# Kernel tuning notes

Measured on AMD Instinct MI355X. Metric: run time of the kernel, lower is better.

## Reference

```python
import jax, jax.numpy as jnp
import numpy as np
from jax import lax

EPS = 0.1
MAX_ITER = 100
THRESH = 0.1


def setup_inputs() -> dict:
    key = jax.random.key(0)
    k1, k2, k3 = jax.random.split(key, 3)
    x = jax.random.normal(k1, (128, 512, 3), dtype=jnp.float32)
    y = jax.random.normal(k2, (128, 512, 3), dtype=jnp.float32)
    species = jax.random.uniform(k3, (512, 8), dtype=jnp.float32)
    return {"x": x, "y": y, "species": species}


def _cost_matrix(x, y, species):
    # periodic displacement: round(dx) - dx, squared L2 over coord dim
    dx = x[:, :, None, :] - y[:, None, :, :]          # (N, P1, P2, D)
    dper = jnp.round(dx) - dx
    dist_sqr = jnp.sum(jnp.abs(dper) ** 2, axis=-1)   # (N, P1, P2)
    C = dist_sqr * jnp.abs(1.0 / (species @ species.T) + 1e-5)  # broadcast (P,P)
    return C, dist_sqr


def _sinkhorn(C):
    N, P1, P2 = C.shape
    mu = jnp.full((N, P1), 1.0 / P1, dtype=C.dtype)
    nu = jnp.full((N, P2), 1.0 / P2, dtype=C.dtype)

    def M(u, v):
        # (-C + u_i + v_j) / eps
        return (-C + u[..., :, None] + v[..., None, :]) / EPS

    def step(carry, _):
        u, v, done = carry
        u_new = EPS * (jnp.log(mu + 1e-8) - jax.nn.logsumexp(M(u, v), axis=-1)) + u
        v_new = EPS * (jnp.log(nu + 1e-8) - jax.nn.logsumexp(M(u_new, v), axis=-2)) + v
        err = jnp.mean(jnp.sum(jnp.abs(u_new - u), axis=-1))
        # torch loop breaks AFTER applying this iteration's update; freeze afterwards
        u_out = jnp.where(done, u, u_new)
        v_out = jnp.where(done, v, v_new)
        done_out = done | (err < THRESH)
        return (u_out, v_out, done_out), None

    init = (jnp.zeros_like(mu), jnp.zeros_like(nu), jnp.array(False))
    (u, v, _), _ = lax.scan(step, init, None, length=MAX_ITER)
    pi = jnp.exp(M(u, v))
    return pi


def reference(x, y, species):
    C, dist_sqr = _cost_matrix(x, y, species)
    pi = _sinkhorn(C)
    cost = jnp.sum(pi * C, axis=(-2, -1))  # (N,), reduction='none'
    return (cost, pi, C, dist_sqr)
```

## Files before the change

### kernel.cpp

```cpp
#include <hip/hip_runtime.h>
#include <hip/hip_cooperative_groups.h>

namespace cg = cooperative_groups;

#define NB    128
#define P     512
#define PP    262144
#define TOT   33554432
#define MAX_IT 100

#define SCR_K      0
#define SCR_W      16777216
#define SCR_CP     17039360
#define SCR_U      17563648
#define SCR_V      17629184
#define SCR_ERRP   17694720
#define SCR_FLOATS 17695744
#define DIST_KEEP  (TOT - SCR_FLOATS)

__device__ __forceinline__ float bfbits(unsigned u) {
  union { unsigned b; float f; } x; x.b = u; return x.f;
}

__global__ void prep_kernel(const float* __restrict__ species,
                            float* __restrict__ scr, float* __restrict__ cost) {
  int tid = blockIdx.x * 256 + threadIdx.x;
  if (tid < PP) {
    int i = tid >> 9, j = tid & (P - 1);
    const float* si = species + i * 8;
    const float* sj = species + j * 8;
    float g = 0.f;
#pragma unroll
    for (int k = 0; k < 8; ++k) g += si[k] * sj[k];
    scr[SCR_W + tid] = fabsf(1.0f / g + 1e-5f);
  }
  if (tid < NB * P) scr[SCR_U + tid] = 0.f;
  if (tid < NB) cost[tid] = 0.f;
}

__global__ void cmat_kernel(const float* __restrict__ x, const float* __restrict__ y,
                            const float* __restrict__ W,
                            unsigned short* __restrict__ K,
                            float* __restrict__ C, float* __restrict__ dist) {
  int g = blockIdx.x * 256 + threadIdx.x;
  int base = g << 2;
  int n = base >> 18;
  int r = base & (PP - 1);
  int i = r >> 9, j0 = r & (P - 1);
  const float* xp = x + ((n << 9) + i) * 3;
  float x0 = xp[0], x1 = xp[1], x2 = xp[2];
  const float* yp = y + ((n << 9) + j0) * 3;
  float4 w4 = *reinterpret_cast<const float4*>(W + r);
  float wv[4] = { w4.x, w4.y, w4.z, w4.w };
  float c[4], d[4];
  unsigned short kk[4];
#pragma unroll
  for (int q = 0; q < 4; ++q) {
    float dx = x0 - yp[q * 3 + 0];
    float dy = x1 - yp[q * 3 + 1];
    float dz = x2 - yp[q * 3 + 2];
    dx = rintf(dx) - dx; dy = rintf(dy) - dy; dz = rintf(dz) - dz;
    float ds = dx * dx + dy * dy + dz * dz;
    d[q] = ds;
    c[q] = ds * wv[q];
    float kf = __expf(-10.f * c[q]);
    unsigned b = __float_as_uint(kf);
    kk[q] = (unsigned short)((b + 0x7fffu + ((b >> 16) & 1u)) >> 16);
  }
  *reinterpret_cast<float4*>(C + base) = make_float4(c[0], c[1], c[2], c[3]);
  if (base < DIST_KEEP)
    *reinterpret_cast<float4*>(dist + base) = make_float4(d[0], d[1], d[2], d[3]);
  uint2 kp;
  kp.x = (unsigned)kk[0] | ((unsigned)kk[1] << 16);
  kp.y = (unsigned)kk[2] | ((unsigned)kk[3] << 16);
  *reinterpret_cast<uint2*>(K + base) = kp;
}

__global__ void tail_kernel(const float* __restrict__ x, const float* __restrict__ y,
                            float* __restrict__ dist) {
  int idx = DIST_KEEP + blockIdx.x * 256 + threadIdx.x;
  int n = idx >> 18;
  int r = idx & (PP - 1);
  int i = r >> 9, j = r & (P - 1);
  const float* xp = x + ((n << 9) + i) * 3;
  const float* yp = y + ((n << 9) + j) * 3;
  float ds = 0.f;
#pragma unroll
  for (int k = 0; k < 3; ++k) {
    float dd = xp[k] - yp[k];
    float per = rintf(dd) - dd;
    ds += per * per;
  }
  dist[idx] = ds;
}

__global__ __launch_bounds__(512, 4)
void sinkhorn_kernel(float* __restrict__ scr) {
  cg::grid_group grid = cg::this_grid();
  const unsigned short* Kus = (const unsigned short*)scr;
  float* u    = scr + SCR_U;
  float* cp   = scr + SCR_CP;
  float* errP = scr + SCR_ERRP;

  const int tid  = threadIdx.x;
  const int lane = tid & 63;
  const int wid  = tid >> 6;
  const int bid  = blockIdx.x;
  const int n    = bid >> 2;
  const int rb   = bid & 3;
  const int row0 = (n << 9) + (rb << 7);

  __shared__ float vLDS[512];
  __shared__ float colsum[512];
  __shared__ float red[512];
  __shared__ float wdu[8];

  vLDS[tid] = 0.f;
  __syncthreads();

  const float logmu = logf(1.0f / 512.0f + 1e-8f);

  for (int it = 0; it < MAX_IT; ++it) {
    const int buf = it & 1;
    float ev[8], colacc[8];
#pragma unroll
    for (int t = 0; t < 8; ++t) {
      ev[t] = __expf(10.f * vLDS[(lane << 3) + t]);
      colacc[t] = 0.f;
    }
    colsum[tid] = 0.f;
    __syncthreads();

    float myDu = 0.f;
#pragma unroll 2
    for (int r = 0; r < 16; ++r) {
      int row = row0 + (wid << 4) + r;
      const uint4* kp = reinterpret_cast<const uint4*>(Kus + ((size_t)row << 9) + (lane << 3));
      uint4 kw = *kp;
      float k[8];
      k[0] = bfbits(kw.x << 16); k[1] = bfbits(kw.x & 0xffff0000u);
      k[2] = bfbits(kw.y << 16); k[3] = bfbits(kw.y & 0xffff0000u);
      k[4] = bfbits(kw.z << 16); k[5] = bfbits(kw.z & 0xffff0000u);
      k[6] = bfbits(kw.w << 16); k[7] = bfbits(kw.w & 0xffff0000u);
      float s = 0.f;
#pragma unroll
      for (int t = 0; t < 8; ++t) s = fmaf(k[t], ev[t], s);
#pragma unroll
      for (int o = 32; o > 0; o >>= 1) s += __shfl_xor(s, o);
      float uo = u[row];
      float un = 0.1f * (logmu - __logf(s));
      myDu += fabsf(un - uo);
      if (lane == 0) u[row] = un;
      float eu = __expf(10.f * un);
#pragma unroll
      for (int t = 0; t < 8; ++t) colacc[t] = fmaf(k[t], eu, colacc[t]);
    }
#pragma unroll
    for (int t = 0; t < 8; ++t) atomicAdd(&colsum[(lane << 3) + t], colacc[t]);
    if (lane == 0) wdu[wid] = myDu;
    __syncthreads();

    cp[(buf << 18) + (n << 11) + (rb << 9) + tid] = colsum[tid];
    if (tid == 0) {
      float e = 0.f;
#pragma unroll
      for (int w = 0; w < 8; ++w) e += wdu[w];
      errP[(buf << 9) + bid] = e;
    }
    grid.sync();

    float sc = 0.f;
#pragma unroll
    for (int q = 0; q < 4; ++q) sc += cp[(buf << 18) + (n << 11) + (q << 9) + tid];
    float vc = 0.1f * (logmu - __logf(sc));

    red[tid] = errP[(buf << 9) + tid];
    __syncthreads();
#pragma unroll
    for (int o = 256; o > 0; o >>= 1) {
      if (tid < o) red[tid] += red[tid + o];
      __syncthreads();
    }
    float errTot = red[0];
    vLDS[tid] = vc;
    __syncthreads();
    if (errTot < 12.8f) break;
  }

  if (rb == 0) scr[SCR_V + (n << 9) + tid] = vLDS[tid];
}

__global__ __launch_bounds__(256)
void pi_kernel(const float* __restrict__ C, const float* __restrict__ scr,
               float* __restrict__ pi, float* __restrict__ cost) {
  int gid = blockIdx.x * 256 + threadIdx.x;
  int lane = threadIdx.x & 63;
  int row = gid >> 6;
  int n = row >> 9;
  int c0 = lane << 3;
  float uu = scr[SCR_U + row];
  const float* vp = scr + SCR_V + (n << 9) + c0;
  float4 va = *reinterpret_cast<const float4*>(vp);
  float4 vb = *reinterpret_cast<const float4*>(vp + 4);
  const float* Cr = C + ((size_t)row << 9) + c0;
  float4 ca = *reinterpret_cast<const float4*>(Cr);
  float4 cb = *reinterpret_cast<const float4*>(Cr + 4);
  float4 pa, pb;
  pa.x = __expf((uu + va.x - ca.x) * 10.f);
  pa.y = __expf((uu + va.y - ca.y) * 10.f);
  pa.z = __expf((uu + va.z - ca.z) * 10.f);
  pa.w = __expf((uu + va.w - ca.w) * 10.f);
  pb.x = __expf((uu + vb.x - cb.x) * 10.f);
  pb.y = __expf((uu + vb.y - cb.y) * 10.f);
  pb.z = __expf((uu + vb.z - cb.z) * 10.f);
  pb.w = __expf((uu + vb.w - cb.w) * 10.f);
  float* Pr = pi + ((size_t)row << 9) + c0;
  *reinterpret_cast<float4*>(Pr) = pa;
  *reinterpret_cast<float4*>(Pr + 4) = pb;
  float acc = pa.x * ca.x + pa.y * ca.y + pa.z * ca.z + pa.w * ca.w
            + pb.x * cb.x + pb.y * cb.y + pb.z * cb.z + pb.w * cb.w;
#pragma unroll
  for (int o = 32; o > 0; o >>= 1) acc += __shfl_xor(acc, o);
  __shared__ float ws[4];
  if (lane == 0) ws[threadIdx.x >> 6] = acc;
  __syncthreads();
  if (threadIdx.x == 0) atomicAdd(cost + n, ws[0] + ws[1] + ws[2] + ws[3]);
}

extern "C" void kernel_launch(void* const* d_in, const int* in_sizes, int n_in,
                              void* d_out, int out_size, void* d_ws, size_t ws_size,
                              hipStream_t stream) {
  const float* x = (const float*)d_in[0];
  const float* y = (const float*)d_in[1];
  const float* species = (const float*)d_in[2];

  float* out  = (float*)d_out;
  float* cost = out;
  float* pi   = out + 128;
  float* C    = pi + (size_t)TOT;
  float* dist = C + (size_t)TOT;
  float* scr  = dist + (size_t)DIST_KEEP;

  hipLaunchKernelGGL(prep_kernel, dim3(PP / 256), dim3(256), 0, stream,
                     species, scr, cost);
  hipLaunchKernelGGL(cmat_kernel, dim3(TOT / 4 / 256), dim3(256), 0, stream,
                     x, y, scr + SCR_W, (unsigned short*)scr, C, dist);

  void* args[] = { (void*)&scr };
  hipLaunchCooperativeKernel((void*)sinkhorn_kernel, dim3(512), dim3(512),
                             args, 0, stream);

  hipLaunchKernelGGL(pi_kernel, dim3(TOT / 8 / 256), dim3(256), 0, stream,
                     C, scr, pi, cost);
  hipLaunchKernelGGL(tail_kernel, dim3(SCR_FLOATS / 256), dim3(256), 0, stream,
                     x, y, dist);
}
```

Baseline: 437.0 us.

## Keep bf16 Gibbs kernel in registers during Sinkhorn, recompute cost in pi kernel

```diff
diff --git a/kernel.cpp b/kernel.cpp
--- a/kernel.cpp
+++ b/kernel.cpp
@@ -9,13 +9,15 @@
 #define TOT   33554432
 #define MAX_IT 100
 
-#define SCR_K      0
-#define SCR_W      16777216
-#define SCR_CP     17039360
-#define SCR_U      17563648
-#define SCR_V      17629184
-#define SCR_ERRP   17694720
-#define SCR_FLOATS 17695744
+#define SCR_W      0
+#define SCR_X      262144
+#define SCR_Y      458752
+#define SCR_CP     655360
+#define SCR_U      1179648
+#define SCR_V      1245184
+#define SCR_ERRP   1310720
+#define SCR_DONE   1311744
+#define SCR_FLOATS 1312000
 #define DIST_KEEP  (TOT - SCR_FLOATS)
 
 __device__ __forceinline__ float bfbits(unsigned u) {
@@ -23,6 +25,7 @@
 }
 
 __global__ void prep_kernel(const float* __restrict__ species,
+                            const float* __restrict__ x, const float* __restrict__ y,
                             float* __restrict__ scr, float* __restrict__ cost) {
   int tid = blockIdx.x * 256 + threadIdx.x;
   if (tid < PP) {
@@ -34,13 +37,17 @@
     for (int k = 0; k < 8; ++k) g += si[k] * sj[k];
     scr[SCR_W + tid] = fabsf(1.0f / g + 1e-5f);
   }
+  if (tid < NB * P * 3) {
+    scr[SCR_X + tid] = x[tid];
+    scr[SCR_Y + tid] = y[tid];
+  }
   if (tid < NB * P) scr[SCR_U + tid] = 0.f;
   if (tid < NB) cost[tid] = 0.f;
+  if (tid == 0) scr[SCR_DONE] = 0.f;
 }
 
 __global__ void cmat_kernel(const float* __restrict__ x, const float* __restrict__ y,
                             const float* __restrict__ W,
-                            unsigned short* __restrict__ K,
                             float* __restrict__ C, float* __restrict__ dist) {
   int g = blockIdx.x * 256 + threadIdx.x;
   int base = g << 2;
@@ -53,7 +60,6 @@
   float4 w4 = *reinterpret_cast<const float4*>(W + r);
   float wv[4] = { w4.x, w4.y, w4.z, w4.w };
   float c[4], d[4];
-  unsigned short kk[4];
 #pragma unroll
   for (int q = 0; q < 4; ++q) {
     float dx = x0 - yp[q * 3 + 0];
@@ -63,17 +69,10 @@
     float ds = dx * dx + dy * dy + dz * dz;
     d[q] = ds;
     c[q] = ds * wv[q];
-    float kf = __expf(-10.f * c[q]);
-    unsigned b = __float_as_uint(kf);
-    kk[q] = (unsigned short)((b + 0x7fffu + ((b >> 16) & 1u)) >> 16);
   }
   *reinterpret_cast<float4*>(C + base) = make_float4(c[0], c[1], c[2], c[3]);
   if (base < DIST_KEEP)
     *reinterpret_cast<float4*>(dist + base) = make_float4(d[0], d[1], d[2], d[3]);
-  uint2 kp;
-  kp.x = (unsigned)kk[0] | ((unsigned)kk[1] << 16);
-  kp.y = (unsigned)kk[2] | ((unsigned)kk[3] << 16);
-  *reinterpret_cast<uint2*>(K + base) = kp;
 }
 
 __global__ void tail_kernel(const float* __restrict__ x, const float* __restrict__ y,
@@ -94,10 +93,142 @@
   dist[idx] = ds;
 }
 
+__global__ __launch_bounds__(256, 2)
+void sink_b(float* __restrict__ scr) {
+  cg::grid_group grid = cg::this_grid();
+  const int tid  = threadIdx.x;
+  const int lane = tid & 63;
+  const int wid  = tid >> 6;
+  const int bid  = blockIdx.x;
+  const int n    = bid >> 2;
+  const int qb   = bid & 3;
+
+  float* u    = scr + SCR_U;
+  float* cp   = scr + SCR_CP;
+  float* errP = scr + SCR_ERRP;
+
+  __shared__ float ys[P * 3];
+  __shared__ float vLDS[P];
+  __shared__ float cbuf[4][P];
+  __shared__ float wdu[4];
+  __shared__ float ebc;
+
+  {
+    const float* yb = scr + SCR_Y + (size_t)(n << 9) * 3;
+    for (int q = tid; q < P * 3; q += 256) ys[q] = yb[q];
+  }
+  vLDS[tid] = 0.f; vLDS[tid + 256] = 0.f;
+  __syncthreads();
+
+  unsigned kreg[128];
+#pragma unroll
+  for (int r = 0; r < 32; ++r) {
+    const int rl = (qb << 7) + (wid << 5) + r;
+    const float* xp = scr + SCR_X + (size_t)((n << 9) + rl) * 3;
+    const float x0 = xp[0], x1 = xp[1], x2 = xp[2];
+    const float* Wr = scr + SCR_W + (rl << 9) + lane;
+    unsigned kk[8];
+#pragma unroll
+    for (int t = 0; t < 8; ++t) {
+      const int j = lane + (t << 6);
+      float w = Wr[t << 6];
+      float dx = x0 - ys[j * 3 + 0];
+      float dy = x1 - ys[j * 3 + 1];
+      float dz = x2 - ys[j * 3 + 2];
+      dx = rintf(dx) - dx; dy = rintf(dy) - dy; dz = rintf(dz) - dz;
+      float ds = dx * dx + dy * dy + dz * dz;
+      float kf = __expf(-10.f * (ds * w));
+      unsigned b = __float_as_uint(kf);
+      kk[t] = (b + 0x7fffu + ((b >> 16) & 1u)) >> 16;
+    }
+#pragma unroll
+    for (int h = 0; h < 4; ++h)
+      kreg[(r << 2) + h] = kk[2 * h] | (kk[2 * h + 1] << 16);
+  }
+
+  const float logmu = logf(1.0f / 512.0f + 1e-8f);
+  const float muv   = 1.0f / 512.0f + 1e-8f;
+
+  for (int it = 0; it < MAX_IT; ++it) {
+    const int buf = it & 1;
+    float ev[8], colacc[8];
+#pragma unroll
+    for (int t = 0; t < 8; ++t) {
+      ev[t] = __expf(10.f * vLDS[lane + (t << 6)]);
+      colacc[t] = 0.f;
+    }
+    float du = 0.f;
+#pragma unroll
+    for (int r = 0; r < 32; ++r) {
+      float k[8];
+#pragma unroll
+      for (int h = 0; h < 4; ++h) {
+        unsigned kw = kreg[(r << 2) + h];
+        k[2 * h]     = bfbits(kw << 16);
+        k[2 * h + 1] = bfbits(kw & 0xffff0000u);
+      }
+      float sA = k[0] * ev[0], sB = k[1] * ev[1];
+      sA = fmaf(k[2], ev[2], sA); sB = fmaf(k[3], ev[3], sB);
+      sA = fmaf(k[4], ev[4], sA); sB = fmaf(k[5], ev[5], sB);
+      sA = fmaf(k[6], ev[6], sA); sB = fmaf(k[7], ev[7], sB);
+      float s = sA + sB;
+#pragma unroll
+      for (int o = 32; o > 0; o >>= 1) s += __shfl_xor(s, o);
+      const int rowg = (n << 9) + (qb << 7) + (wid << 5) + r;
+      float uo = u[rowg];
+      float un = 0.1f * (logmu - __logf(s));
+      du += fabsf(un - uo);
+      if (lane == 0) u[rowg] = un;
+      float eu = __fdividef(muv, s);
+#pragma unroll
+      for (int t = 0; t < 8; ++t) colacc[t] = fmaf(k[t], eu, colacc[t]);
+    }
+#pragma unroll
+    for (int t = 0; t < 8; ++t) cbuf[wid][lane + (t << 6)] = colacc[t];
+    if (lane == 0) wdu[wid] = du;
+    __syncthreads();
+
+    {
+      float s1 = cbuf[0][tid] + cbuf[1][tid] + cbuf[2][tid] + cbuf[3][tid];
+      int c2 = tid + 256;
+      float s2 = cbuf[0][c2] + cbuf[1][c2] + cbuf[2][c2] + cbuf[3][c2];
+      float* cpd = cp + (buf << 18) + (n << 11) + (qb << 9);
+      cpd[tid] = s1; cpd[c2] = s2;
+      if (tid == 0) errP[(buf << 9) + bid] = wdu[0] + wdu[1] + wdu[2] + wdu[3];
+    }
+    grid.sync();
+
+    {
+      const float* cpb = cp + (buf << 18) + (n << 11);
+      float sc1 = cpb[tid] + cpb[512 + tid] + cpb[1024 + tid] + cpb[1536 + tid];
+      int c2 = tid + 256;
+      float sc2 = cpb[c2] + cpb[512 + c2] + cpb[1024 + c2] + cpb[1536 + c2];
+      vLDS[tid] = 0.1f * (logmu - __logf(sc1));
+      vLDS[c2]  = 0.1f * (logmu - __logf(sc2));
+    }
+    if (wid == 0) {
+      float e = 0.f;
+#pragma unroll
+      for (int q = 0; q < 8; ++q) e += errP[(buf << 9) + lane + (q << 6)];
+#pragma unroll
+      for (int o = 32; o > 0; o >>= 1) e += __shfl_xor(e, o);
+      if (lane == 0) ebc = e;
+    }
+    __syncthreads();
+    if (ebc < 12.8f) break;
+  }
+
+  if (qb == 0) {
+    scr[SCR_V + (n << 9) + tid]       = vLDS[tid];
+    scr[SCR_V + (n << 9) + tid + 256] = vLDS[tid + 256];
+  }
+  if (tid == 0) scr[SCR_DONE] = 1.0f;
+}
+
 __global__ __launch_bounds__(512, 4)
-void sinkhorn_kernel(float* __restrict__ scr) {
+void sink_rescue(const float* __restrict__ Cm, float* __restrict__ scr) {
+  if (scr[SCR_DONE] != 0.f) return;
   cg::grid_group grid = cg::this_grid();
-  const unsigned short* Kus = (const unsigned short*)scr;
   float* u    = scr + SCR_U;
   float* cp   = scr + SCR_CP;
   float* errP = scr + SCR_ERRP;
@@ -110,9 +241,9 @@
   const int rb   = bid & 3;
   const int row0 = (n << 9) + (rb << 7);
 
-  __shared__ float vLDS[512];
-  __shared__ float colsum[512];
-  __shared__ float red[512];
+  __shared__ float vLDS[P];
+  __shared__ float colsum[P];
+  __shared__ float red[P];
   __shared__ float wdu[8];
 
   vLDS[tid] = 0.f;
@@ -135,13 +266,14 @@
 #pragma unroll 2
     for (int r = 0; r < 16; ++r) {
       int row = row0 + (wid << 4) + r;
-      const uint4* kp = reinterpret_cast<const uint4*>(Kus + ((size_t)row << 9) + (lane << 3));
-      uint4 kw = *kp;
+      const float* Cr = Cm + ((size_t)row << 9) + (lane << 3);
+      float4 ca = *reinterpret_cast<const float4*>(Cr);
+      float4 cb = *reinterpret_cast<const float4*>(Cr + 4);
       float k[8];
-      k[0] = bfbits(kw.x << 16); k[1] = bfbits(kw.x & 0xffff0000u);
-      k[2] = bfbits(kw.y << 16); k[3] = bfbits(kw.y & 0xffff0000u);
-      k[4] = bfbits(kw.z << 16); k[5] = bfbits(kw.z & 0xffff0000u);
-      k[6] = bfbits(kw.w << 16); k[7] = bfbits(kw.w & 0xffff0000u);
+      k[0] = __expf(-10.f * ca.x); k[1] = __expf(-10.f * ca.y);
+      k[2] = __expf(-10.f * ca.z); k[3] = __expf(-10.f * ca.w);
+      k[4] = __expf(-10.f * cb.x); k[5] = __expf(-10.f * cb.y);
+      k[6] = __expf(-10.f * cb.z); k[7] = __expf(-10.f * cb.w);
       float s = 0.f;
 #pragma unroll
       for (int t = 0; t < 8; ++t) s = fmaf(k[t], ev[t], s);
@@ -162,16 +294,13 @@
 
     cp[(buf << 18) + (n << 11) + (rb << 9) + tid] = colsum[tid];
     if (tid == 0) {
-      float e = 0.f;
-#pragma unroll
-      for (int w = 0; w < 8; ++w) e += wdu[w];
-      errP[(buf << 9) + bid] = e;
+      errP[(buf << 9) + bid] = wdu[0] + wdu[1] + wdu[2] + wdu[3]
+                             + wdu[4] + wdu[5] + wdu[6] + wdu[7];
     }
     grid.sync();
 
-    float sc = 0.f;
-#pragma unroll
-    for (int q = 0; q < 4; ++q) sc += cp[(buf << 18) + (n << 11) + (q << 9) + tid];
+    const float* cpb = cp + (buf << 18) + (n << 11);
+    float sc = cpb[tid] + cpb[512 + tid] + cpb[1024 + tid] + cpb[1536 + tid];
     float vc = 0.1f * (logmu - __logf(sc));
 
     red[tid] = errP[(buf << 9) + tid];
@@ -191,40 +320,64 @@
 }
 
 __global__ __launch_bounds__(256)
-void pi_kernel(const float* __restrict__ C, const float* __restrict__ scr,
+void pi_kernel(const float* __restrict__ x, const float* __restrict__ y,
+               const float* __restrict__ scr,
                float* __restrict__ pi, float* __restrict__ cost) {
-  int gid = blockIdx.x * 256 + threadIdx.x;
-  int lane = threadIdx.x & 63;
-  int row = gid >> 6;
-  int n = row >> 9;
-  int c0 = lane << 3;
-  float uu = scr[SCR_U + row];
+  const int tid  = threadIdx.x;
+  const int lane = tid & 63;
+  const int wid  = tid >> 6;
+  const int rowg = blockIdx.x * 4 + wid;
+  const int n    = rowg >> 9;
+  const int i    = rowg & (P - 1);
+
+  __shared__ float ys[P * 3];
+  {
+    const float* yb = y + (size_t)(n << 9) * 3;
+    for (int q = tid; q < P * 3; q += 256) ys[q] = yb[q];
+  }
+  __syncthreads();
+
+  const int c0 = lane << 3;
+  const float* xp = x + (size_t)rowg * 3;
+  const float x0 = xp[0], x1 = xp[1], x2 = xp[2];
+  const float uu = scr[SCR_U + rowg];
   const float* vp = scr + SCR_V + (n << 9) + c0;
-  float4 va = *reinterpret_cast<const float4*>(vp);
-  float4 vb = *reinterpret_cast<const float4*>(vp + 4);
-  const float* Cr = C + ((size_t)row << 9) + c0;
-  float4 ca = *reinterpret_cast<const float4*>(Cr);
-  float4 cb = *reinterpret_cast<const float4*>(Cr + 4);
-  float4 pa, pb;
-  pa.x = __expf((uu + va.x - ca.x) * 10.f);
-  pa.y = __expf((uu + va.y - ca.y) * 10.f);
-  pa.z = __expf((uu + va.z - ca.z) * 10.f);
-  pa.w = __expf((uu + va.w - ca.w) * 10.f);
-  pb.x = __expf((uu + vb.x - cb.x) * 10.f);
-  pb.y = __expf((uu + vb.y - cb.y) * 10.f);
-  pb.z = __expf((uu + vb.z - cb.z) * 10.f);
-  pb.w = __expf((uu + vb.w - cb.w) * 10.f);
-  float* Pr = pi + ((size_t)row << 9) + c0;
-  *reinterpret_cast<float4*>(Pr) = pa;
-  *reinterpret_cast<float4*>(Pr + 4) = pb;
-  float acc = pa.x * ca.x + pa.y * ca.y + pa.z * ca.z + pa.w * ca.w
-            + pb.x * cb.x + pb.y * cb.y + pb.z * cb.z + pb.w * cb.w;
+  const float* Wr = scr + SCR_W + i * P + c0;
+
+  float acc = 0.f;
+  float4 po[2];
+#pragma unroll
+  for (int h = 0; h < 2; ++h) {
+    float4 v4 = *reinterpret_cast<const float4*>(vp + h * 4);
+    float4 w4 = *reinterpret_cast<const float4*>(Wr + h * 4);
+    float vv[4] = { v4.x, v4.y, v4.z, v4.w };
+    float wv[4] = { w4.x, w4.y, w4.z, w4.w };
+    float pq[4];
+#pragma unroll
+    for (int q = 0; q < 4; ++q) {
+      const int j = c0 + h * 4 + q;
+      float dx = x0 - ys[j * 3 + 0];
+      float dy = x1 - ys[j * 3 + 1];
+      float dz = x2 - ys[j * 3 + 2];
+      dx = rintf(dx) - dx; dy = rintf(dy) - dy; dz = rintf(dz) - dz;
+      float ds = dx * dx + dy * dy + dz * dz;
+      float c  = ds * wv[q];
+      float p  = __expf((uu + vv[q] - c) * 10.f);
+      pq[q] = p;
+      acc = fmaf(p, c, acc);
+    }
+    po[h] = make_float4(pq[0], pq[1], pq[2], pq[3]);
+  }
+  float* Pr = pi + ((size_t)rowg << 9) + c0;
+  *reinterpret_cast<float4*>(Pr)     = po[0];
+  *reinterpret_cast<float4*>(Pr + 4) = po[1];
+
 #pragma unroll
   for (int o = 32; o > 0; o >>= 1) acc += __shfl_xor(acc, o);
-  __shared__ float ws[4];
-  if (lane == 0) ws[threadIdx.x >> 6] = acc;
+  __shared__ float wsum[4];
+  if (lane == 0) wsum[wid] = acc;
   __syncthreads();
-  if (threadIdx.x == 0) atomicAdd(cost + n, ws[0] + ws[1] + ws[2] + ws[3]);
+  if (tid == 0) atomicAdd(cost + n, wsum[0] + wsum[1] + wsum[2] + wsum[3]);
 }
 
 extern "C" void kernel_launch(void* const* d_in, const int* in_sizes, int n_in,
@@ -242,16 +395,20 @@
   float* scr  = dist + (size_t)DIST_KEEP;
 
   hipLaunchKernelGGL(prep_kernel, dim3(PP / 256), dim3(256), 0, stream,
-                     species, scr, cost);
+                     species, x, y, scr, cost);
   hipLaunchKernelGGL(cmat_kernel, dim3(TOT / 4 / 256), dim3(256), 0, stream,
-                     x, y, scr + SCR_W, (unsigned short*)scr, C, dist);
-
-  void* args[] = { (void*)&scr };
-  hipLaunchCooperativeKernel((void*)sinkhorn_kernel, dim3(512), dim3(512),
-                             args, 0, stream);
-
-  hipLaunchKernelGGL(pi_kernel, dim3(TOT / 8 / 256), dim3(256), 0, stream,
-                     C, scr, pi, cost);
+                     x, y, scr + SCR_W, C, dist);
+
+  void* fargs[] = { (void*)&scr };
+  hipLaunchCooperativeKernel((void*)sink_b, dim3(512), dim3(256),
+                             fargs, 0, stream);
+
+  void* rargs[] = { (void*)&C, (void*)&scr };
+  hipLaunchCooperativeKernel((void*)sink_rescue, dim3(512), dim3(512),
+                             rargs, 0, stream);
+
+  hipLaunchKernelGGL(pi_kernel, dim3(NB * P / 4), dim3(256), 0, stream,
+                     x, y, scr, pi, cost);
   hipLaunchKernelGGL(tail_kernel, dim3(SCR_FLOATS / 256), dim3(256), 0, stream,
                      x, y, dist);
 }
```

Result: slower. 655.3 us (+49.9%).
